# Optimization experiments

Hardware: AMD Instinct MI355X
Metric: run time of the kernel (lower is better)

The kernel has to match this reference:

```python
import jax, jax.numpy as jnp
import numpy as np

N_NODES = 50000
N_EDGES = 800000
FEAT = 10
HID = 64
N_SHEETS = 256
SHEET_LEN = 128
NUM_GRAPHS = 1


def _glorot(key, shape):
    fan_in, fan_out = shape[0], shape[1]
    lim = float(np.sqrt(6.0 / (fan_in + fan_out)))
    return jax.random.uniform(key, shape, jnp.float32, -lim, lim)


def setup_inputs() -> dict:
    key = jax.random.key(0)
    ks = jax.random.split(key, 16)
    x = jax.random.normal(ks[0], (N_NODES, FEAT), jnp.float32)
    edge_index = jax.random.randint(ks[1], (2, N_EDGES), 0, N_NODES, jnp.int64)
    batch = jnp.zeros((N_NODES,), jnp.int64)
    sheet_node_idx = jax.random.randint(ks[2], (N_SHEETS, SHEET_LEN), 0, N_NODES, jnp.int64)
    sheet_features = jax.random.normal(ks[3], (N_SHEETS, FEAT), jnp.float32)
    return {
        "x": x, "edge_index": edge_index, "batch": batch,
        "sheet_node_idx": sheet_node_idx, "sheet_features": sheet_features,
        "W_gcn1": _glorot(ks[4], (FEAT, HID)), "b_gcn1": jnp.zeros((HID,), jnp.float32),
        "W_gcn2": _glorot(ks[5], (HID, HID)), "b_gcn2": jnp.zeros((HID,), jnp.float32),
        "W_gcn3": _glorot(ks[6], (HID, HID)), "b_gcn3": jnp.zeros((HID,), jnp.float32),
        "geo_W1": _glorot(ks[7], (FEAT, HID)), "geo_b1": jnp.zeros((HID,), jnp.float32),
        "geo_W2": _glorot(ks[8], (HID, HID)), "geo_b2": jnp.zeros((HID,), jnp.float32),
        "fus_W": _glorot(ks[9], (2 * HID, HID)), "fus_b": jnp.zeros((HID,), jnp.float32),
        "q_W1": _glorot(ks[10], (2 * HID, HID)), "q_b1": jnp.zeros((HID,), jnp.float32),
        "q_W2": _glorot(ks[11], (HID, 1)), "q_b2": jnp.zeros((1,), jnp.float32),
    }


def gcn_conv(x, W, b, src, dst, norm_edge, norm_self):
    # PyG GCNConv: h = x @ W, symmetric-normalized aggregation with self loops, + b
    h = x @ W                                  # [N, H]
    msg = h[src] * norm_edge[:, None]          # [E, H] gather
    agg = jax.ops.segment_sum(msg, dst, num_segments=x.shape[0])  # scatter-add
    agg = agg + h * norm_self[:, None]         # self-loop contribution
    return agg + b


def reference(x, edge_index, batch, sheet_node_idx, sheet_features,
              W_gcn1, b_gcn1, W_gcn2, b_gcn2, W_gcn3, b_gcn3,
              geo_W1, geo_b1, geo_W2, geo_b2, fus_W, fus_b,
              q_W1, q_b1, q_W2, q_b2):
    src, dst = edge_index[0], edge_index[1]
    N = x.shape[0]
    # degree with self loops (edge weights = 1), counted on destination
    deg = jax.ops.segment_sum(jnp.ones_like(dst, jnp.float32), dst, num_segments=N) + 1.0
    dinv = jax.lax.rsqrt(deg)
    norm_edge = dinv[src] * dinv[dst]   # [E]
    norm_self = dinv * dinv             # [N]

    h = jax.nn.relu(gcn_conv(x, W_gcn1, b_gcn1, src, dst, norm_edge, norm_self))
    h = jax.nn.relu(gcn_conv(h, W_gcn2, b_gcn2, src, dst, norm_edge, norm_self))
    h = jax.nn.relu(gcn_conv(h, W_gcn3, b_gcn3, src, dst, norm_edge, norm_self))

    # global mean pool over batch ids (single graph here)
    sums = jax.ops.segment_sum(h, batch, num_segments=NUM_GRAPHS)
    counts = jax.ops.segment_sum(jnp.ones((N,), jnp.float32), batch, num_segments=NUM_GRAPHS)
    g_emb = sums / counts[:, None]      # [1, H]

    # per-sheet mean pooling (equal-length sheets)
    sheet_embs = h[sheet_node_idx].mean(axis=1)            # [S, H]

    geo = jax.nn.relu(sheet_features @ geo_W1 + geo_b1) @ geo_W2 + geo_b2
    fused = jax.nn.relu(jnp.concatenate([sheet_embs, geo], axis=1) @ fus_W + fus_b)

    global_embs = jnp.broadcast_to(g_emb, (fused.shape[0], g_emb.shape[1]))
    hq = jnp.concatenate([fused, global_embs], axis=1)
    q = jax.nn.relu(hq @ q_W1 + q_b1) @ q_W2 + q_b2
    return q[:, 0]
```

## Files before the change

### kernel.cpp

```cpp
#include <hip/hip_runtime.h>

#define HID 64
#define FEAT 10
#define MAXSEG 8192

typedef unsigned short u16;

__device__ __forceinline__ u16 f2bf(float f) {
    unsigned u = __float_as_uint(f);
    unsigned r = (u + 0x7fffu + ((u >> 16) & 1u)) >> 16;
    return (u16)r;
}
__device__ __forceinline__ void bf8_add(float* acc, uint4 u) {
    acc[0] += __uint_as_float(u.x << 16);
    acc[1] += __uint_as_float(u.x & 0xffff0000u);
    acc[2] += __uint_as_float(u.y << 16);
    acc[3] += __uint_as_float(u.y & 0xffff0000u);
    acc[4] += __uint_as_float(u.z << 16);
    acc[5] += __uint_as_float(u.z & 0xffff0000u);
    acc[6] += __uint_as_float(u.w << 16);
    acc[7] += __uint_as_float(u.w & 0xffff0000u);
}

template<int RS>
__device__ __forceinline__ void gather_rows(float* acc, const u16* __restrict__ base,
                                            const u16* __restrict__ csr2,
                                            int i0, int cnt, int c0) {
    int trips = cnt >> 3;
    if (!trips) return;
    int last = i0 + cnt - 8;
    uint4 evA = *(const uint4*)(csr2 + i0);
    uint4 evB = *(const uint4*)(csr2 + (trips > 1 ? i0 + 8 : i0));
    int j = 0;
    for (; j + 2 <= trips; j += 2) {
        int inA = i0 + 8 * (j + 2); if (inA > last) inA = last;
        int inB = inA + 8;          if (inB > last) inB = last;
        uint4 evA2 = *(const uint4*)(csr2 + inA);
        uint4 evB2 = *(const uint4*)(csr2 + inB);
        uint4 a0 = *(const uint4*)(base + (size_t)(evA.x & 0xffff) * RS + c0);
        uint4 a1 = *(const uint4*)(base + (size_t)(evA.x >> 16)    * RS + c0);
        uint4 a2 = *(const uint4*)(base + (size_t)(evA.y & 0xffff) * RS + c0);
        uint4 a3 = *(const uint4*)(base + (size_t)(evA.y >> 16)    * RS + c0);
        uint4 a4 = *(const uint4*)(base + (size_t)(evA.z & 0xffff) * RS + c0);
        uint4 a5 = *(const uint4*)(base + (size_t)(evA.z >> 16)    * RS + c0);
        uint4 a6 = *(const uint4*)(base + (size_t)(evA.w & 0xffff) * RS + c0);
        uint4 a7 = *(const uint4*)(base + (size_t)(evA.w >> 16)    * RS + c0);
        uint4 b0 = *(const uint4*)(base + (size_t)(evB.x & 0xffff) * RS + c0);
        uint4 b1 = *(const uint4*)(base + (size_t)(evB.x >> 16)    * RS + c0);
        uint4 b2 = *(const uint4*)(base + (size_t)(evB.y & 0xffff) * RS + c0);
        uint4 b3 = *(const uint4*)(base + (size_t)(evB.y >> 16)    * RS + c0);
        uint4 b4 = *(const uint4*)(base + (size_t)(evB.z & 0xffff) * RS + c0);
        uint4 b5 = *(const uint4*)(base + (size_t)(evB.z >> 16)    * RS + c0);
        uint4 b6 = *(const uint4*)(base + (size_t)(evB.w & 0xffff) * RS + c0);
        uint4 b7 = *(const uint4*)(base + (size_t)(evB.w >> 16)    * RS + c0);
        bf8_add(acc, a0); bf8_add(acc, a1); bf8_add(acc, a2); bf8_add(acc, a3);
        bf8_add(acc, a4); bf8_add(acc, a5); bf8_add(acc, a6); bf8_add(acc, a7);
        bf8_add(acc, b0); bf8_add(acc, b1); bf8_add(acc, b2); bf8_add(acc, b3);
        bf8_add(acc, b4); bf8_add(acc, b5); bf8_add(acc, b6); bf8_add(acc, b7);
        evA = evA2; evB = evB2;
    }
    if (j < trips) {
        uint4 a0 = *(const uint4*)(base + (size_t)(evA.x & 0xffff) * RS + c0);
        uint4 a1 = *(const uint4*)(base + (size_t)(evA.x >> 16)    * RS + c0);
        uint4 a2 = *(const uint4*)(base + (size_t)(evA.y & 0xffff) * RS + c0);
        uint4 a3 = *(const uint4*)(base + (size_t)(evA.y >> 16)    * RS + c0);
        uint4 a4 = *(const uint4*)(base + (size_t)(evA.z & 0xffff) * RS + c0);
        uint4 a5 = *(const uint4*)(base + (size_t)(evA.z >> 16)    * RS + c0);
        uint4 a6 = *(const uint4*)(base + (size_t)(evA.w & 0xffff) * RS + c0);
        uint4 a7 = *(const uint4*)(base + (size_t)(evA.w >> 16)    * RS + c0);
        bf8_add(acc, a0); bf8_add(acc, a1); bf8_add(acc, a2); bf8_add(acc, a3);
        bf8_add(acc, a4); bf8_add(acc, a5); bf8_add(acc, a6); bf8_add(acc, a7);
    }
}


__global__ __launch_bounds__(1024) void bin_kernel(
        const int* __restrict__ src, const int* __restrict__ dst,
        int* __restrict__ gcnt, unsigned* __restrict__ tmp,
        u16* __restrict__ hwba, u16* __restrict__ hwbb, u16* __restrict__ xp,
        int E, int N) {
    __shared__ int h[256];
    int t = threadIdx.x, c = blockIdx.x;
    if (t < 256) h[t] = 0;
    __syncthreads();
    int b0 = c * 4096;
    unsigned pk[4]; int bk[4];
    #pragma unroll
    for (int j = 0; j < 4; j++) {
        int e = b0 + t + j * 1024;
        if (e < E) {
            int s = src[e], d = dst[e];
            pk[j] = ((unsigned)(d & 255) << 16) | (unsigned)s;
            bk[j] = d >> 8;
            atomicAdd(&h[bk[j]], 1);
        } else bk[j] = -1;
    }
    __syncthreads();
    if (t < 256) {
        int v = h[t];
        int resv = v ? atomicAdd(&gcnt[t], v) : 0;
        h[t] = t * MAXSEG + resv;
    }
    __syncthreads();
    #pragma unroll
    for (int j = 0; j < 4; j++) {
        if (bk[j] >= 0) {
            int slot = atomicAdd(&h[bk[j]], 1);
            tmp[slot] = pk[j];
        }
    }
    if (c == 0) {
        if (t < 64)       hwba[(size_t)N * 64 + t] = 0;
        else if (t < 128) hwbb[(size_t)N * 64 + (t - 64)] = 0;
        else if (t < 144) xp[(size_t)N * 16 + (t - 128)] = 0;
    }
}

__global__ __launch_bounds__(1024) void csr_build(
        const unsigned* __restrict__ tmp, const int* __restrict__ gcnt,
        u16* __restrict__ csr2,
        int* __restrict__ row_start, int* __restrict__ row_cntp,
        float* __restrict__ dinv,
        const float* __restrict__ x, u16* __restrict__ xp, int N) {
    __shared__ __align__(16) u16 staged[MAXSEG];
    __shared__ int cntL[256], padL[256], scanL[256], curL[256];
    __shared__ float sdinv[256];
    int b = blockIdx.x, t = threadIdx.x;
    if (t < 256) cntL[t] = 0;
    for (int i = t; i < MAXSEG; i += 1024) staged[i] = (u16)N;
    __syncthreads();
    int segBase = b * MAXSEG, segLen = gcnt[b];
    for (int i = t; i < segLen; i += 1024)
        atomicAdd(&cntL[tmp[segBase + i] >> 16], 1);
    __syncthreads();
    if (t < 256) { padL[t] = (cntL[t] + 7) & ~7; scanL[t] = padL[t]; }
    __syncthreads();
    for (int off = 1; off < 256; off <<= 1) {
        int a = (t < 256) ? scanL[t] : 0;
        int s = (t >= off && t < 256) ? scanL[t - off] : 0;
        __syncthreads();
        if (t < 256) scanL[t] = a + s;
        __syncthreads();
    }
    if (t < 256) {
        int excl = scanL[t] - padL[t];
        curL[t] = excl;
        float dv = rsqrtf((float)cntL[t] + 1.0f);
        sdinv[t] = dv;
        int node = b * 256 + t;
        if (node < N) {
            row_start[node] = b * MAXSEG + excl;
            row_cntp[node]  = padL[t];
            dinv[node]      = dv;
        }
    }
    __syncthreads();
    for (int i = t; i < segLen; i += 1024) {
        unsigned e = tmp[segBase + i];
        int idx = atomicAdd(&curL[e >> 16], 1);
        staged[idx] = (u16)(e & 0xffffu);
    }
    for (int i = t; i < 256 * 16; i += 1024) {
        int nlc = i >> 4, cch = i & 15;
        int node = b * 256 + nlc;
        if (node < N)
            xp[(size_t)node * 16 + cch] =
                (cch < FEAT) ? f2bf(sdinv[nlc] * x[(size_t)node * FEAT + cch]) : (u16)0;
    }
    __syncthreads();
    ((uint4*)(csr2 + (size_t)b * MAXSEG))[t] = ((const uint4*)staged)[t];
}


__global__ __launch_bounds__(256) void l1l2(
        const int* __restrict__ row_start, const int* __restrict__ row_cntp,
        const u16* __restrict__ csr2, const u16* __restrict__ xp,
        const float* __restrict__ dinv,
        const float* __restrict__ W1, const float* __restrict__ b1,
        const float* __restrict__ W2,
        u16* __restrict__ hwba, int N) {
    __shared__ float sW[64 * 64];
    __shared__ float sH16[64 * 16];
    __shared__ float sH64[64 * 65];
    int t = threadIdx.x;
    int node0 = blockIdx.x * 64;
    for (int i = t; i < FEAT * 64; i += 256) sW[i] = W1[i];
    if (t < 128) {
        int nl = t >> 1;
        int node = node0 + nl;
        int c0 = (t & 1) * 8;
        float acc[8] = {0.f,0.f,0.f,0.f,0.f,0.f,0.f,0.f};
        if (node < N) {
            uint4 sv = *(const uint4*)(xp + (size_t)node * 16 + c0);
            bf8_add(acc, sv);
            gather_rows<16>(acc, xp, csr2, row_start[node], row_cntp[node], c0);
            float di = dinv[node];
            #pragma unroll
            for (int j = 0; j < 8; j++) acc[j] *= di;
        }
        #pragma unroll
        for (int j = 0; j < 8; j++) sH16[nl * 16 + c0 + j] = acc[j];
    }
    __syncthreads();
    int c0 = (t & 15) * 4;
    int rbase = (t >> 4) * 4;
    {
        float4 a0 = {0,0,0,0}, a1 = {0,0,0,0}, a2 = {0,0,0,0}, a3 = {0,0,0,0};
        for (int k = 0; k < FEAT; k++) {
            float4 w = *(const float4*)(sW + k * 64 + c0);
            float h0 = sH16[(rbase + 0) * 16 + k];
            float h1v = sH16[(rbase + 1) * 16 + k];
            float h2 = sH16[(rbase + 2) * 16 + k];
            float h3 = sH16[(rbase + 3) * 16 + k];
            a0.x += h0 * w.x; a0.y += h0 * w.y; a0.z += h0 * w.z; a0.w += h0 * w.w;
            a1.x += h1v * w.x; a1.y += h1v * w.y; a1.z += h1v * w.z; a1.w += h1v * w.w;
            a2.x += h2 * w.x; a2.y += h2 * w.y; a2.z += h2 * w.z; a2.w += h2 * w.w;
            a3.x += h3 * w.x; a3.y += h3 * w.y; a3.z += h3 * w.z; a3.w += h3 * w.w;
        }
        float4 bb = *(const float4*)(b1 + c0);
        float4 accs[4] = {a0, a1, a2, a3};
        #pragma unroll
        for (int rr = 0; rr < 4; rr++) {
            float4 v = accs[rr];
            int r = rbase + rr;
            sH64[r * 65 + c0 + 0] = fmaxf(v.x + bb.x, 0.f);
            sH64[r * 65 + c0 + 1] = fmaxf(v.y + bb.y, 0.f);
            sH64[r * 65 + c0 + 2] = fmaxf(v.z + bb.z, 0.f);
            sH64[r * 65 + c0 + 3] = fmaxf(v.w + bb.w, 0.f);
        }
    }
    __syncthreads();
    for (int i = t * 4; i < 4096; i += 256 * 4)
        *(float4*)(sW + i) = *(const float4*)(W2 + i);
    __syncthreads();
    {
        float4 a0 = {0,0,0,0}, a1 = {0,0,0,0}, a2 = {0,0,0,0}, a3 = {0,0,0,0};
        for (int k = 0; k < 64; k++) {
            float4 w = *(const float4*)(sW + k * 64 + c0);
            float h0 = sH64[(rbase + 0) * 65 + k];
            float h1v = sH64[(rbase + 1) * 65 + k];
            float h2 = sH64[(rbase + 2) * 65 + k];
            float h3 = sH64[(rbase + 3) * 65 + k];
            a0.x += h0 * w.x; a0.y += h0 * w.y; a0.z += h0 * w.z; a0.w += h0 * w.w;
            a1.x += h1v * w.x; a1.y += h1v * w.y; a1.z += h1v * w.z; a1.w += h1v * w.w;
            a2.x += h2 * w.x; a2.y += h2 * w.y; a2.z += h2 * w.z; a2.w += h2 * w.w;
            a3.x += h3 * w.x; a3.y += h3 * w.y; a3.z += h3 * w.z; a3.w += h3 * w.w;
        }
        float4 accs[4] = {a0, a1, a2, a3};
        for (int rr = 0; rr < 4; rr++) {
            int node = node0 + rbase + rr;
            if (node >= N) break;
            float di = dinv[node];
            float4 v = accs[rr];
            ushort4 o;
            o.x = f2bf(v.x * di); o.y = f2bf(v.y * di);
            o.z = f2bf(v.z * di); o.w = f2bf(v.w * di);
            *(ushort4*)(hwba + (size_t)node * 64 + c0) = o;
        }
    }
}


__global__ __launch_bounds__(512) void g2l3(
        const int* __restrict__ row_start, const int* __restrict__ row_cntp,
        const u16* __restrict__ csr2, const u16* __restrict__ hwba,
        const float* __restrict__ dinv, const float* __restrict__ b2,
        const float* __restrict__ W3,
        u16* __restrict__ hwbb, int N) {
    __shared__ float sW[64 * 64];
    __shared__ float sH64[64 * 65];
    int t = threadIdx.x;
    int node0 = blockIdx.x * 64;
    {
        int nl = t >> 3;
        int node = node0 + nl;
        int c0 = (t & 7) * 8;
        float acc[8] = {0.f,0.f,0.f,0.f,0.f,0.f,0.f,0.f};
        if (node < N) {
            uint4 sv = *(const uint4*)(hwba + (size_t)node * 64 + c0);
            bf8_add(acc, sv);
            gather_rows<64>(acc, hwba, csr2, row_start[node], row_cntp[node], c0);
            float di = dinv[node];
            const float4 bb0 = *(const float4*)(b2 + c0);
            const float4 bb1 = *(const float4*)(b2 + c0 + 4);
            acc[0] = fmaxf(acc[0]*di + bb0.x, 0.f); acc[1] = fmaxf(acc[1]*di + bb0.y, 0.f);
            acc[2] = fmaxf(acc[2]*di + bb0.z, 0.f); acc[3] = fmaxf(acc[3]*di + bb0.w, 0.f);
            acc[4] = fmaxf(acc[4]*di + bb1.x, 0.f); acc[5] = fmaxf(acc[5]*di + bb1.y, 0.f);
            acc[6] = fmaxf(acc[6]*di + bb1.z, 0.f); acc[7] = fmaxf(acc[7]*di + bb1.w, 0.f);
        }
        #pragma unroll
        for (int j = 0; j < 8; j++) sH64[nl * 65 + c0 + j] = acc[j];
    }
    for (int i = t * 4; i < 4096; i += 512 * 4)
        *(float4*)(sW + i) = *(const float4*)(W3 + i);
    __syncthreads();
    {
        int c0 = (t & 15) * 4;
        int r0 = (t >> 4) * 2;
        float4 a0 = {0,0,0,0}, a1 = {0,0,0,0};
        for (int k = 0; k < 64; k++) {
            float4 w = *(const float4*)(sW + k * 64 + c0);
            float h0 = sH64[(r0 + 0) * 65 + k];
            float h1v = sH64[(r0 + 1) * 65 + k];
            a0.x += h0 * w.x; a0.y += h0 * w.y; a0.z += h0 * w.z; a0.w += h0 * w.w;
            a1.x += h1v * w.x; a1.y += h1v * w.y; a1.z += h1v * w.z; a1.w += h1v * w.w;
        }
        float4 accs[2] = {a0, a1};
        for (int rr = 0; rr < 2; rr++) {
            int node = node0 + r0 + rr;
            if (node >= N) break;
            float di = dinv[node];
            float4 v = accs[rr];
            ushort4 o;
            o.x = f2bf(v.x * di); o.y = f2bf(v.y * di);
            o.z = f2bf(v.z * di); o.w = f2bf(v.w * di);
            *(ushort4*)(hwbb + (size_t)node * 64 + c0) = o;
        }
    }
}


__global__ __launch_bounds__(256) void gather_b3(
        const int* __restrict__ row_start, const int* __restrict__ row_cntp,
        const u16* __restrict__ csr2, const u16* __restrict__ hwbb,
        const float* __restrict__ dinv, const float* __restrict__ b,
        float* __restrict__ out, float* __restrict__ part, int N) {
    int t = threadIdx.x;
    int nl = t >> 3;
    int node = blockIdx.x * 32 + nl;
    int c0 = (t & 7) * 8;
    float acc[8] = {0.f,0.f,0.f,0.f,0.f,0.f,0.f,0.f};
    if (node < N) {
        uint4 sv = *(const uint4*)(hwbb + (size_t)node * 64 + c0);
        bf8_add(acc, sv);
        gather_rows<64>(acc, hwbb, csr2, row_start[node], row_cntp[node], c0);
        float di = dinv[node];
        const float4 bb0 = *(const float4*)(b + c0);
        const float4 bb1 = *(const float4*)(b + c0 + 4);
        float4 o0, o1;
        o0.x = fmaxf(acc[0]*di + bb0.x, 0.f); o0.y = fmaxf(acc[1]*di + bb0.y, 0.f);
        o0.z = fmaxf(acc[2]*di + bb0.z, 0.f); o0.w = fmaxf(acc[3]*di + bb0.w, 0.f);
        o1.x = fmaxf(acc[4]*di + bb1.x, 0.f); o1.y = fmaxf(acc[5]*di + bb1.y, 0.f);
        o1.z = fmaxf(acc[6]*di + bb1.z, 0.f); o1.w = fmaxf(acc[7]*di + bb1.w, 0.f);
        *(float4*)(out + (size_t)node * 64 + c0)     = o0;
        *(float4*)(out + (size_t)node * 64 + c0 + 4) = o1;
        acc[0]=o0.x; acc[1]=o0.y; acc[2]=o0.z; acc[3]=o0.w;
        acc[4]=o1.x; acc[5]=o1.y; acc[6]=o1.z; acc[7]=o1.w;
    }
    __shared__ float red[32 * 64];
    #pragma unroll
    for (int j = 0; j < 8; j++) red[nl * 64 + c0 + j] = acc[j];
    __syncthreads();
    if (t < 64) {
        float s = 0.f;
        #pragma unroll 8
        for (int k = 0; k < 32; k++) s += red[k * 64 + t];
        part[(size_t)blockIdx.x * 64 + t] = s;
    }
}

__global__ __launch_bounds__(64) void gsum_reduce(const float* __restrict__ part,
                                                  float* __restrict__ gsum, int NB) {
    int c = blockIdx.x, t = threadIdx.x;
    float s = 0.f;
    for (int i = t; i < NB; i += 64) s += part[(size_t)i * 64 + c];
    for (int off = 32; off > 0; off >>= 1) s += __shfl_down(s, off, 64);
    if (t == 0) gsum[c] = s;
}


__global__ __launch_bounds__(256) void final_kernel(
        const float* __restrict__ h3, const int* __restrict__ sheet_idx,
        const float* __restrict__ sheet_feat, const float* __restrict__ g_sum,
        const float* __restrict__ gW1, const float* __restrict__ gb1,
        const float* __restrict__ gW2, const float* __restrict__ gb2,
        const float* __restrict__ fW,  const float* __restrict__ fb,
        const float* __restrict__ qW1, const float* __restrict__ qb1,
        const float* __restrict__ qW2, const float* __restrict__ qb2,
        float* __restrict__ out, int N, int L) {
    int s = blockIdx.x, t = threadIdx.x;
    __shared__ float red[256];
    __shared__ float semb[64];
    __shared__ float geoh[64];
    __shared__ float geo[64];
    __shared__ float hq[128];
    int c = t & 63, jg = t >> 6;
    float acc = 0.0f;
    for (int j = jg; j < L; j += 4) {
        int node = sheet_idx[s * L + j];
        acc += h3[(size_t)node * 64 + c];
    }
    red[t] = acc;
    __syncthreads();
    if (t < 64) {
        semb[t] = (red[t] + red[t + 64] + red[t + 128] + red[t + 192]) / (float)L;
        hq[64 + t] = g_sum[t] / (float)N;
        float a = gb1[t];
        #pragma unroll
        for (int k = 0; k < FEAT; k++) a += sheet_feat[s * FEAT + k] * gW1[k * 64 + t];
        geoh[t] = fmaxf(a, 0.0f);
    }
    __syncthreads();
    if (t < 64) {
        float a = gb2[t];
        for (int k = 0; k < 64; k++) a += geoh[k] * gW2[k * 64 + t];
        geo[t] = a;
    }
    __syncthreads();
    if (t < 64) {
        float a = fb[t];
        for (int k = 0; k < 64; k++) a += semb[k] * fW[k * 64 + t];
        for (int k = 0; k < 64; k++) a += geo[k]  * fW[(64 + k) * 64 + t];
        hq[t] = fmaxf(a, 0.0f);
    }
    __syncthreads();
    float q = 0.0f;
    if (t < 64) {
        float a = qb1[t];
        for (int k = 0; k < 128; k++) a += hq[k] * qW1[k * 64 + t];
        a = fmaxf(a, 0.0f);
        q = a * qW2[t];
        for (int off = 32; off > 0; off >>= 1) q += __shfl_down(q, off, 64);
        if (t == 0) out[s] = q + qb2[0];
    }
}

extern "C" void kernel_launch(void* const* d_in, const int* in_sizes, int n_in,
                              void* d_out, int out_size, void* d_ws, size_t ws_size,
                              hipStream_t stream) {
    const float* x          = (const float*)d_in[0];
    const int*   edge       = (const int*)d_in[1];
    const int*   sheet_idx  = (const int*)d_in[3];
    const float* sheet_feat = (const float*)d_in[4];
    const float* W1 = (const float*)d_in[5];  const float* b1 = (const float*)d_in[6];
    const float* W2 = (const float*)d_in[7];  const float* b2 = (const float*)d_in[8];
    const float* W3 = (const float*)d_in[9];  const float* b3 = (const float*)d_in[10];
    const float* gW1 = (const float*)d_in[11]; const float* gb1 = (const float*)d_in[12];
    const float* gW2 = (const float*)d_in[13]; const float* gb2 = (const float*)d_in[14];
    const float* fW  = (const float*)d_in[15]; const float* fb  = (const float*)d_in[16];
    const float* qW1 = (const float*)d_in[17]; const float* qb1 = (const float*)d_in[18];
    const float* qW2 = (const float*)d_in[19]; const float* qb2 = (const float*)d_in[20];
    float* out = (float*)d_out;

    int N = in_sizes[2];
    int E = in_sizes[1] / 2;
    int S = in_sizes[4] / FEAT;
    int L = in_sizes[3] / S;

    int nbuckets = (N + 255) / 256;
    int nchunks  = (E + 4095) / 4096;

    int gMM = (N + 63) / 64;
    int gGB = (N + 31) / 32;

    char* p = (char*)d_ws;
    unsigned* tmp  = (unsigned*)p;             p += (size_t)nbuckets * MAXSEG * 4;
    u16* csr2      = (u16*)p;                  p += (size_t)nbuckets * MAXSEG * 2;
    float* hf      = (float*)p;                p += (size_t)N * 64 * 4;
    u16* hwba      = (u16*)p;                  p += (size_t)(N + 1) * 64 * 2;
    u16* hwbb      = (u16*)p;                  p += (size_t)(N + 1) * 64 * 2;
    u16* xp        = (u16*)p;                  p += (size_t)(N + 1) * 16 * 2;
    int* row_start = (int*)p;                  p += (size_t)N * 4;
    int* row_cntp  = (int*)p;                  p += (size_t)N * 4;
    float* dinv    = (float*)p;                p += (size_t)N * 4;
    float* part    = (float*)p;                p += (size_t)gGB * 64 * 4;
    int* gcnt      = (int*)p;                  p += 256 * 4;
    float* gsum    = (float*)p;                p += 64 * 4;

    hipMemsetAsync(gcnt, 0, 256 * 4, stream);

    const int* src = edge;
    const int* dst = edge + E;

    bin_kernel<<<nchunks, 1024, 0, stream>>>(src, dst, gcnt, tmp, hwba, hwbb, xp, E, N);
    csr_build<<<nbuckets, 1024, 0, stream>>>(tmp, gcnt, csr2, row_start, row_cntp, dinv, x, xp, N);

    l1l2<<<gMM, 256, 0, stream>>>(row_start, row_cntp, csr2, xp, dinv, W1, b1, W2, hwba, N);
    g2l3<<<gMM, 512, 0, stream>>>(row_start, row_cntp, csr2, hwba, dinv, b2, W3, hwbb, N);
    gather_b3<<<gGB, 256, 0, stream>>>(row_start, row_cntp, csr2, hwbb, dinv, b3, hf, part, N);
    gsum_reduce<<<64, 64, 0, stream>>>(part, gsum, gGB);

    final_kernel<<<S, 256, 0, stream>>>(hf, sheet_idx, sheet_feat, gsum,
                                        gW1, gb1, gW2, gb2, fW, fb,
                                        qW1, qb1, qW2, qb2, out, N, L);
}
```

Before: 220.1 us.

## Use bf16 MFMA for 64x64 dense transforms in layer kernels

Replaces the scalar FP32 64x64 matmuls in l1l2 and g2l3 with bf16 MFMA 16x16x32 instructions. Hidden activations are stored in shared memory as bf16 with a padded stride, and W2/W3 are transposed and converted to bf16 in shared memory. dinv values are cached in shared memory. This is meant to cut ALU time and LDS traffic in these kernels. In exchange, the matmul inputs lose precision and the output stores become scattered 2-byte writes.

```diff
diff --git a/kernel.cpp b/kernel.cpp
--- a/kernel.cpp
+++ b/kernel.cpp
@@ -3,8 +3,11 @@
 #define HID 64
 #define FEAT 10
 #define MAXSEG 8192
+#define HSTR 72
 
 typedef unsigned short u16;
+typedef __attribute__((ext_vector_type(8))) short bf16x8;
+typedef __attribute__((ext_vector_type(4))) float f32x4;
 
 __device__ __forceinline__ u16 f2bf(float f) {
     unsigned u = __float_as_uint(f);
@@ -179,12 +182,19 @@
         const float* __restrict__ W1, const float* __restrict__ b1,
         const float* __restrict__ W2,
         u16* __restrict__ hwba, int N) {
-    __shared__ float sW[64 * 64];
+    __shared__ float sW1[FEAT * 64];
     __shared__ float sH16[64 * 16];
-    __shared__ float sH64[64 * 65];
+    __shared__ __align__(16) u16 sHbf[64 * HSTR];
+    __shared__ __align__(16) u16 sWT[64 * HSTR];
+    __shared__ float sdv[64];
     int t = threadIdx.x;
     int node0 = blockIdx.x * 64;
-    for (int i = t; i < FEAT * 64; i += 256) sW[i] = W1[i];
+    for (int i = t; i < FEAT * 64; i += 256) sW1[i] = W1[i];
+    for (int i = t; i < 4096; i += 256) {
+        int k = i >> 6, c = i & 63;
+        sWT[c * HSTR + k] = f2bf(W2[i]);
+    }
+    if (t < 64) sdv[t] = (node0 + t < N) ? dinv[node0 + t] : 0.f;
     if (t < 128) {
         int nl = t >> 1;
         int node = node0 + nl;
@@ -207,7 +217,7 @@
     {
         float4 a0 = {0,0,0,0}, a1 = {0,0,0,0}, a2 = {0,0,0,0}, a3 = {0,0,0,0};
         for (int k = 0; k < FEAT; k++) {
-            float4 w = *(const float4*)(sW + k * 64 + c0);
+            float4 w = *(const float4*)(sW1 + k * 64 + c0);
             float h0 = sH16[(rbase + 0) * 16 + k];
             float h1v = sH16[(rbase + 1) * 16 + k];
             float h2 = sH16[(rbase + 2) * 16 + k];
@@ -223,39 +233,43 @@
         for (int rr = 0; rr < 4; rr++) {
             float4 v = accs[rr];
             int r = rbase + rr;
-            sH64[r * 65 + c0 + 0] = fmaxf(v.x + bb.x, 0.f);
-            sH64[r * 65 + c0 + 1] = fmaxf(v.y + bb.y, 0.f);
-            sH64[r * 65 + c0 + 2] = fmaxf(v.z + bb.z, 0.f);
-            sH64[r * 65 + c0 + 3] = fmaxf(v.w + bb.w, 0.f);
-        }
-    }
-    __syncthreads();
-    for (int i = t * 4; i < 4096; i += 256 * 4)
-        *(float4*)(sW + i) = *(const float4*)(W2 + i);
+            ushort4 o;
+            o.x = f2bf(fmaxf(v.x + bb.x, 0.f));
+            o.y = f2bf(fmaxf(v.y + bb.y, 0.f));
+            o.z = f2bf(fmaxf(v.z + bb.z, 0.f));
+            o.w = f2bf(fmaxf(v.w + bb.w, 0.f));
+            *(ushort4*)(sHbf + r * HSTR + c0) = o;
+        }
+    }
     __syncthreads();
     {
-        float4 a0 = {0,0,0,0}, a1 = {0,0,0,0}, a2 = {0,0,0,0}, a3 = {0,0,0,0};
-        for (int k = 0; k < 64; k++) {
-            float4 w = *(const float4*)(sW + k * 64 + c0);
-            float h0 = sH64[(rbase + 0) * 65 + k];
-            float h1v = sH64[(rbase + 1) * 65 + k];
-            float h2 = sH64[(rbase + 2) * 65 + k];
-            float h3 = sH64[(rbase + 3) * 65 + k];
-            a0.x += h0 * w.x; a0.y += h0 * w.y; a0.z += h0 * w.z; a0.w += h0 * w.w;
-            a1.x += h1v * w.x; a1.y += h1v * w.y; a1.z += h1v * w.z; a1.w += h1v * w.w;
-            a2.x += h2 * w.x; a2.y += h2 * w.y; a2.z += h2 * w.z; a2.w += h2 * w.w;
-            a3.x += h3 * w.x; a3.y += h3 * w.y; a3.z += h3 * w.z; a3.w += h3 * w.w;
-        }
-        float4 accs[4] = {a0, a1, a2, a3};
-        for (int rr = 0; rr < 4; rr++) {
-            int node = node0 + rbase + rr;
-            if (node >= N) break;
-            float di = dinv[node];
-            float4 v = accs[rr];
-            ushort4 o;
-            o.x = f2bf(v.x * di); o.y = f2bf(v.y * di);
-            o.z = f2bf(v.z * di); o.w = f2bf(v.w * di);
-            *(ushort4*)(hwba + (size_t)node * 64 + c0) = o;
+        int lane = t & 63, w = t >> 6;
+        int cl = lane & 15, g = lane >> 4;
+        f32x4 ac0 = {0,0,0,0}, ac1 = {0,0,0,0}, ac2 = {0,0,0,0}, ac3 = {0,0,0,0};
+        const u16* arow = sHbf + (16 * w + cl) * HSTR;
+        #pragma unroll
+        for (int kh = 0; kh < 2; kh++) {
+            bf16x8 a  = *(const bf16x8*)(arow + kh * 32 + g * 8);
+            bf16x8 f0 = *(const bf16x8*)(sWT + (cl)      * HSTR + kh * 32 + g * 8);
+            bf16x8 f1 = *(const bf16x8*)(sWT + (16 + cl) * HSTR + kh * 32 + g * 8);
+            bf16x8 f2 = *(const bf16x8*)(sWT + (32 + cl) * HSTR + kh * 32 + g * 8);
+            bf16x8 f3 = *(const bf16x8*)(sWT + (48 + cl) * HSTR + kh * 32 + g * 8);
+            ac0 = __builtin_amdgcn_mfma_f32_16x16x32_bf16(a, f0, ac0, 0, 0, 0);
+            ac1 = __builtin_amdgcn_mfma_f32_16x16x32_bf16(a, f1, ac1, 0, 0, 0);
+            ac2 = __builtin_amdgcn_mfma_f32_16x16x32_bf16(a, f2, ac2, 0, 0, 0);
+            ac3 = __builtin_amdgcn_mfma_f32_16x16x32_bf16(a, f3, ac3, 0, 0, 0);
+        }
+        int r0 = 16 * w + 4 * g;
+        #pragma unroll
+        for (int reg = 0; reg < 4; reg++) {
+            int node = node0 + r0 + reg;
+            if (node < N) {
+                float dv = sdv[r0 + reg];
+                hwba[(size_t)node * 64 +  0 + cl] = f2bf(ac0[reg] * dv);
+                hwba[(size_t)node * 64 + 16 + cl] = f2bf(ac1[reg] * dv);
+                hwba[(size_t)node * 64 + 32 + cl] = f2bf(ac2[reg] * dv);
+                hwba[(size_t)node * 64 + 48 + cl] = f2bf(ac3[reg] * dv);
+            }
         }
     }
 }
@@ -267,8 +281,9 @@
         const float* __restrict__ dinv, const float* __restrict__ b2,
         const float* __restrict__ W3,
         u16* __restrict__ hwbb, int N) {
-    __shared__ float sW[64 * 64];
-    __shared__ float sH64[64 * 65];
+    __shared__ __align__(16) u16 sHbf[64 * HSTR];
+    __shared__ __align__(16) u16 sWT[64 * HSTR];
+    __shared__ float sdv[64];
     int t = threadIdx.x;
     int node0 = blockIdx.x * 64;
     {
@@ -288,33 +303,42 @@
             acc[4] = fmaxf(acc[4]*di + bb1.x, 0.f); acc[5] = fmaxf(acc[5]*di + bb1.y, 0.f);
             acc[6] = fmaxf(acc[6]*di + bb1.z, 0.f); acc[7] = fmaxf(acc[7]*di + bb1.w, 0.f);
         }
-        #pragma unroll
-        for (int j = 0; j < 8; j++) sH64[nl * 65 + c0 + j] = acc[j];
-    }
-    for (int i = t * 4; i < 4096; i += 512 * 4)
-        *(float4*)(sW + i) = *(const float4*)(W3 + i);
+        ushort4 lo, hi;
+        lo.x = f2bf(acc[0]); lo.y = f2bf(acc[1]); lo.z = f2bf(acc[2]); lo.w = f2bf(acc[3]);
+        hi.x = f2bf(acc[4]); hi.y = f2bf(acc[5]); hi.z = f2bf(acc[6]); hi.w = f2bf(acc[7]);
+        *(ushort4*)(sHbf + nl * HSTR + c0)     = lo;
+        *(ushort4*)(sHbf + nl * HSTR + c0 + 4) = hi;
+    }
+    for (int i = t; i < 4096; i += 512) {
+        int k = i >> 6, c = i & 63;
+        sWT[c * HSTR + k] = f2bf(W3[i]);
+    }
+    if (t < 64) sdv[t] = (node0 + t < N) ? dinv[node0 + t] : 0.f;
     __syncthreads();
     {
-        int c0 = (t & 15) * 4;
-        int r0 = (t >> 4) * 2;
-        float4 a0 = {0,0,0,0}, a1 = {0,0,0,0};
-        for (int k = 0; k < 64; k++) {
-            float4 w = *(const float4*)(sW + k * 64 + c0);
-            float h0 = sH64[(r0 + 0) * 65 + k];
-            float h1v = sH64[(r0 + 1) * 65 + k];
-            a0.x += h0 * w.x; a0.y += h0 * w.y; a0.z += h0 * w.z; a0.w += h0 * w.w;
-            a1.x += h1v * w.x; a1.y += h1v * w.y; a1.z += h1v * w.z; a1.w += h1v * w.w;
-        }
-        float4 accs[2] = {a0, a1};
-        for (int rr = 0; rr < 2; rr++) {
-            int node = node0 + r0 + rr;
-            if (node >= N) break;
-            float di = dinv[node];
-            float4 v = accs[rr];
-            ushort4 o;
-            o.x = f2bf(v.x * di); o.y = f2bf(v.y * di);
-            o.z = f2bf(v.z * di); o.w = f2bf(v.w * di);
-            *(ushort4*)(hwbb + (size_t)node * 64 + c0) = o;
+        int lane = t & 63, w = t >> 6;
+        int cl = lane & 15, g = lane >> 4;
+        int strip = w >> 1;
+        int tb = (w & 1) * 2;
+        f32x4 acA = {0,0,0,0}, acB = {0,0,0,0};
+        const u16* arow = sHbf + (16 * strip + cl) * HSTR;
+        #pragma unroll
+        for (int kh = 0; kh < 2; kh++) {
+            bf16x8 a  = *(const bf16x8*)(arow + kh * 32 + g * 8);
+            bf16x8 fA = *(const bf16x8*)(sWT + (16 * tb       + cl) * HSTR + kh * 32 + g * 8);
+            bf16x8 fB = *(const bf16x8*)(sWT + (16 * (tb + 1) + cl) * HSTR + kh * 32 + g * 8);
+            acA = __builtin_amdgcn_mfma_f32_16x16x32_bf16(a, fA, acA, 0, 0, 0);
+            acB = __builtin_amdgcn_mfma_f32_16x16x32_bf16(a, fB, acB, 0, 0, 0);
+        }
+        int r0 = 16 * strip + 4 * g;
+        #pragma unroll
+        for (int reg = 0; reg < 4; reg++) {
+            int node = node0 + r0 + reg;
+            if (node < N) {
+                float dv = sdv[r0 + reg];
+                hwbb[(size_t)node * 64 + 16 * tb       + cl] = f2bf(acA[reg] * dv);
+                hwbb[(size_t)node * 64 + 16 * (tb + 1) + cl] = f2bf(acB[reg] * dv);
+            }
         }
     }
 }
```

New measurement: 193.6 us. 12.0% less time.
